# Kernel tuning notes

Hardware: AMD Instinct MI355X
Metric: run time of the kernel (lower is better)

The kernel has to match this reference:

```python
import jax, jax.numpy as jnp
import numpy as np

EMBED_DIM = 768
NUM_HEADS = 12
EPS = 1e-6


def setup_inputs() -> dict:
    key = jax.random.key(0)
    ks = jax.random.split(key, 9)
    B, C, H, W = 8, EMBED_DIM, 48, 48
    std = 0.02
    E = EMBED_DIM
    return {
        "query": jax.random.normal(ks[0], (B, C, H, W), dtype=jnp.float32),
        "Wq": jax.random.normal(ks[1], (E, E), dtype=jnp.float32) * std,
        "bq": jnp.zeros((E,), dtype=jnp.float32),
        "Wk": jax.random.normal(ks[2], (E, E), dtype=jnp.float32) * std,
        "bk": jnp.zeros((E,), dtype=jnp.float32),
        "Wv": jax.random.normal(ks[3], (E, E), dtype=jnp.float32) * std,
        "bv": jnp.zeros((E,), dtype=jnp.float32),
        "Wo": jax.random.normal(ks[4], (E, E), dtype=jnp.float32) * std,
        "bo": jnp.zeros((E,), dtype=jnp.float32),
    }


def reference(query, Wq, bq, Wk, bk, Wv, bv, Wo, bo):
    # query: (B, C, H, W) -> (L, B, E) with L = H*W
    B, C, H, W = query.shape
    L = H * W
    E = C
    h = NUM_HEADS
    d = E // h
    x = query.reshape(B, C, L).transpose(2, 0, 1)  # (L, B, E)

    # cos/sin positional reweighting: pi/2 * (i+1) / L
    idx = (jnp.pi / 2) * jnp.arange(1, L + 1, dtype=x.dtype) / L
    sin = jnp.sin(idx)[None, :, None]  # (1, L, 1)
    cos = jnp.cos(idx)[None, :, None]

    # projections + relu feature map
    q = jax.nn.relu(x @ Wq.T + bq)
    k = jax.nn.relu(x @ Wk.T + bk)
    v = x @ Wv.T + bv

    def to_heads(t):  # (L, B, E) -> (B*h, L, d)
        return t.reshape(L, B * h, d).transpose(1, 0, 2)

    q, k, v = to_heads(q), to_heads(k), to_heads(v)

    q_ = jnp.concatenate([q * sin, q * cos], axis=-1)  # (n, L, 2d)
    k_ = jnp.concatenate([k * sin, k * cos], axis=-1)

    # non-causal linear attention
    kv = jnp.einsum("nld,nlm->ndm", k_, v)              # (n, 2d, d)
    z = 1.0 / jnp.maximum(jnp.einsum("nld,nd->nl", q_, k_.sum(axis=1)), EPS)
    out = jnp.einsum("nld,ndm,nl->nlm", q_, kv, z)       # (n, L, d)

    # residual (DropPath is identity at inference)
    attn = x + out.transpose(1, 0, 2).reshape(L, B, E)
    return attn @ Wo.T + bo
```

## Files before the change

### kernel.cpp

```cpp
#include <hip/hip_runtime.h>


#define L_SEQ 2304
#define BATCH 8
#define EDIM 768
#define NHEAD 12
#define DHEAD 64
#define MROWS (L_SEQ * BATCH)

typedef __attribute__((ext_vector_type(8))) short bf16x8_t;
typedef __attribute__((ext_vector_type(4))) float f32x4_t;

__device__ __forceinline__ float b2f(unsigned short u) {
  union { unsigned int i; float f; } x; x.i = ((unsigned int)u) << 16; return x.f;
}
__device__ __forceinline__ unsigned short f2b(float f) {
  union { float f; unsigned int i; } x; x.f = f;
  unsigned int r = x.i + 0x7FFFu + ((x.i >> 16) & 1u);
  return (unsigned short)(r >> 16);
}

#define GLOAD_LDS16(g, l)                                                     \
  __builtin_amdgcn_global_load_lds(                                           \
      (const __attribute__((address_space(1))) unsigned int*)(g),             \
      (__attribute__((address_space(3))) unsigned int*)(l), 16, 0, 0)

__global__ __launch_bounds__(256) void prep(
    const float* __restrict__ q,
    const float* __restrict__ W0, const float* __restrict__ W1,
    const float* __restrict__ W2, const float* __restrict__ W3,
    unsigned short* __restrict__ wbf, unsigned short* __restrict__ xT,
    float* __restrict__ kvz, float2* __restrict__ sct) {
  __shared__ float tile[64][65];
  int bx = blockIdx.x;
  int t = threadIdx.x;
  if (bx < 2304) {
    int y = bx / 576;
    const float* W = (y == 0) ? W0 : (y == 1) ? W1 : (y == 2) ? W2 : W3;
    unsigned short* d = wbf + (size_t)y * EDIM * EDIM;
    int idx = (bx - y * 576) * 256 + t;
    float4 v = *(const float4*)(W + (size_t)idx * 4);
    ushort4 o;
    o.x = f2b(v.x); o.y = f2b(v.y); o.z = f2b(v.z); o.w = f2b(v.w);
    *(ushort4*)(d + (size_t)idx * 4) = o;
  } else if (bx < 5760) {
    int bb = bx - 2304;
    int e0 = (bb % 12) * 64;
    int l0 = ((bb / 12) % 36) * 64;
    int b = bb / 432;
    int li = t & 63, er = t >> 6;
#pragma unroll
    for (int p = 0; p < 16; p++) {
      int eo = er + p * 4;
      tile[eo][li] = q[((size_t)b * EDIM + (e0 + eo)) * L_SEQ + (l0 + li)];
    }
    __syncthreads();
    int ei = t & 63, lr = t >> 6;
#pragma unroll
    for (int p = 0; p < 16; p++) {
      int lo = lr + p * 4;
      xT[((size_t)b * L_SEQ + (l0 + lo)) * EDIM + (e0 + ei)] = f2b(tile[ei][lo]);
    }
  } else if (bx < 6540) {
    int idx = (bx - 5760) * 256 + t;
    *(float4*)(kvz + (size_t)idx * 4) = make_float4(0.f, 0.f, 0.f, 0.f);
  } else {
    int l = (bx - 6540) * 256 + t;
    if (l < L_SEQ) {
      float sv, cv;
      sincosf(1.5707963267948966f * (float)(l + 1) / 2304.0f, &sv, &cv);
      sct[l] = make_float2(sv, cv);
    }
  }
}

#define ABUF(b_) ((b_) * 8192)
#define BBUF(b_) (16384 + (b_) * 8192)

#define BAR() __builtin_amdgcn_s_barrier()
#define SB0() __builtin_amdgcn_sched_barrier(0)
#define LGKM0() asm volatile("s_waitcnt lgkmcnt(0)")
#define VMW(N) asm volatile("s_waitcnt vmcnt(" #N ")" ::: "memory")

#define STG_AB(kt_, B_)                                                       \
  {                                                                           \
    GLOAD_LDS16(a_sb + (size_t)(kt_) * 64, lds + ABUF(B_) + t * 8);           \
    GLOAD_LDS16(a_sb + (size_t)64 * EDIM + (size_t)(kt_) * 64,                \
                lds + ABUF(B_) + 4096 + t * 8);                               \
    GLOAD_LDS16(b_sb + (size_t)(kt_) * 64, lds + BBUF(B_) + t * 8);           \
    GLOAD_LDS16(b_sb + (size_t)64 * EDIM + (size_t)(kt_) * 64,                \
                lds + BBUF(B_) + 4096 + t * 8);                               \
  }

#define DS_RD(B_)                                                             \
  _Pragma("unroll") for (int m_ = 0; m_ < 4; m_++)                            \
  _Pragma("unroll") for (int kk_ = 0; kk_ < 2; kk_++)                         \
    aF[m_][kk_] = *(const bf16x8_t*)(lds + ABUF(B_) +                         \
        ((a_base + (m_ >> 1) * 4096 + (m_ & 1) * 1024 + kk_ * 32) ^ xorv));   \
  _Pragma("unroll") for (int n_ = 0; n_ < 2; n_++)                            \
  _Pragma("unroll") for (int kk_ = 0; kk_ < 2; kk_++)                         \
    bF[n_][kk_] = *(const bf16x8_t*)(lds + BBUF(B_) +                         \
        ((b_base + n_ * 4096 + kk_ * 32) ^ xorv));

#define MFMA16()                                                              \
  __builtin_amdgcn_s_setprio(1);                                              \
  _Pragma("unroll") for (int m_ = 0; m_ < 4; m_++)                            \
  _Pragma("unroll") for (int n_ = 0; n_ < 2; n_++)                            \
  _Pragma("unroll") for (int kk_ = 0; kk_ < 2; kk_++)                         \
    acc[m_][n_] = __builtin_amdgcn_mfma_f32_16x16x32_bf16(                    \
        aF[m_][kk_], bF[n_][kk_], acc[m_][n_], 0, 0, 0);                      \
  __builtin_amdgcn_s_setprio(0);

template <int MODE>
__global__ __launch_bounds__(512, 4) void gemm256(
    const unsigned short* __restrict__ A,
    const unsigned short* __restrict__ Wall,
    const float* __restrict__ bias0, const float* __restrict__ bias1,
    const float* __restrict__ bias2,
    unsigned short* __restrict__ dst0, unsigned short* __restrict__ dst1,
    unsigned short* __restrict__ dst2,
    float* __restrict__ dstf) {
  extern __shared__ __align__(16) unsigned short lds[];

  const unsigned short* W;
  const float* bias;
  unsigned short* dst = nullptr;
  bool do_relu = false;
  int rowblk, colblk;
  {
    int nwg = (int)gridDim.x;
    int wg = ((int)blockIdx.x & 7) * (nwg >> 3) + ((int)blockIdx.x >> 3);
    if (MODE == 0) {
      rowblk = wg / 18;
      int c = wg - rowblk * 18;
      colblk = c % 6;
      int z = c / 6;
      W = Wall + (size_t)z * EDIM * EDIM;
      bias = (z == 0) ? bias0 : (z == 1) ? bias1 : bias2;
      dst = (z == 0) ? dst0 : (z == 1) ? dst1 : dst2;
      do_relu = (z < 2);
    } else {
      rowblk = wg / 6;
      colblk = wg - rowblk * 6;
      W = Wall;
      bias = bias0;
    }
  }
  const int row0 = rowblk * 128;
  const int col0 = colblk * 128;

  const int t = threadIdx.x;
  const int lane = t & 63;
  const int wave = t >> 6;
  const int wm = wave >> 2;
  const int wn = wave & 3;
  const int mrow = lane & 15;
  const int quad = lane >> 4;

  const int xorv = (mrow & 7) << 3;
  const int a_base = (wm * 32 + mrow) * 64 + quad * 8;
  const int b_base = (wn * 16 + mrow) * 64 + quad * 8;

  const int lr_s = t >> 3;
  const int k0_s = ((((t >> 3) & 7) ^ (t & 7)) << 3);
  const unsigned short* a_sb = A + (size_t)(row0 + lr_s) * EDIM + k0_s;
  const unsigned short* b_sb = W + (size_t)(col0 + lr_s) * EDIM + k0_s;

  f32x4_t acc[4][2] = {};
  bf16x8_t aF[4][2], bF[2][2];

  STG_AB(0, 0);
  STG_AB(1, 1);
  VMW(4);
  BAR();

#pragma unroll
  for (int i = 0; i < 12; ++i) {
    const int cur = i & 1;
    DS_RD(cur);
    SB0();
    LGKM0();
    BAR();
    if (i < 10) STG_AB(i + 2, cur);
    MFMA16();
    if (i < 10) { VMW(4); } else { VMW(0); }
    BAR();
  }

  const int bb = row0 / L_SEQ;
#pragma unroll
  for (int ti = 0; ti < 4; ti++) {
    int rbase = row0 + (ti >> 1) * 64 + wm * 32 + (ti & 1) * 16 + quad * 4;
#pragma unroll
    for (int tj = 0; tj < 2; tj++) {
      int gc = col0 + tj * 64 + wn * 16 + mrow;
      float bv = bias[gc];
#pragma unroll
      for (int r = 0; r < 4; r++) {
        int gr = rbase + r;
        float v = acc[ti][tj][r] + bv;
        if (MODE == 0) {
          if (do_relu) v = fmaxf(v, 0.0f);
          int ll = gr - bb * L_SEQ;
          int n = bb * NHEAD + (gc >> 6);
          dst[((size_t)n * L_SEQ + ll) * DHEAD + (gc & 63)] = f2b(v);
        } else {
          dstf[(size_t)gr * EDIM + gc] = v;
        }
      }
    }
  }
}

__global__ __launch_bounds__(256) void kv_mfma(
    const unsigned short* __restrict__ kbuf, const unsigned short* __restrict__ vbuf,
    const float2* __restrict__ sct,
    float* __restrict__ kvT, float* __restrict__ ksum) {
  constexpr int ST = 40;
  __shared__ __align__(16) unsigned short ksT[128 * ST];
  __shared__ __align__(16) unsigned short vsT[64 * ST];
  __shared__ float ksum_l[128];
  int n = blockIdx.x;
  int lbase = blockIdx.y * 288;
  int t = threadIdx.x;
  int lane = t & 63, wave = t >> 6;
  int mrow = lane & 15, quad = lane >> 4;

  if (t < 128) ksum_l[t] = 0.f;

  int lrd = t >> 3;
  int oct = t & 7;
  int col2 = (lrd + ((oct & 3) << 3)) & 31;
  const unsigned short* kbase = kbuf + (size_t)n * L_SEQ * DHEAD + oct * 8;
  const unsigned short* vbase = vbuf + (size_t)n * L_SEQ * DHEAD + oct * 8;

  int rv = wave * 16 + mrow;
  const unsigned short* vrd = vsT + rv * ST + (((quad + (rv >> 3)) & 3) << 3);

  f32x4_t acc[8] = {};
  float sks[8] = {}, skc[8] = {};

  for (int s = 0; s < 9; s++) {
    int l = lbase + s * 32 + lrd;
    float2 sc = sct[l];
    union { uint4 q; unsigned short u[8]; } kq, vq;
    kq.q = *(const uint4*)(kbase + (size_t)l * DHEAD);
    vq.q = *(const uint4*)(vbase + (size_t)l * DHEAD);
    __syncthreads();
#pragma unroll
    for (int e = 0; e < 8; e++) {
      int d = oct * 8 + e;
      float kval = b2f(kq.u[e]);
      float a = kval * sc.x, c = kval * sc.y;
      ksT[d * ST + col2] = f2b(a);
      ksT[(64 + d) * ST + col2] = f2b(c);
      vsT[d * ST + col2] = vq.u[e];
      sks[e] += a;
      skc[e] += c;
    }
    __syncthreads();
    bf16x8_t af = *(const bf16x8_t*)(vrd);
#pragma unroll
    for (int jt = 0; jt < 8; jt++) {
      int rk = jt * 16 + mrow;
      bf16x8_t bfk = *(const bf16x8_t*)(ksT + rk * ST + (((quad + (rk >> 3)) & 3) << 3));
      acc[jt] = __builtin_amdgcn_mfma_f32_16x16x32_bf16(af, bfk, acc[jt], 0, 0, 0);
    }
  }

#pragma unroll
  for (int e = 0; e < 8; e++) {
    atomicAdd(&ksum_l[oct * 8 + e], sks[e]);
    atomicAdd(&ksum_l[64 + oct * 8 + e], skc[e]);
  }
  __syncthreads();
  if (t < 128) atomicAdd(&ksum[n * 128 + t], ksum_l[t]);

#pragma unroll
  for (int jt = 0; jt < 8; jt++) {
#pragma unroll
    for (int r = 0; r < 4; r++) {
      int m = wave * 16 + quad * 4 + r;
      int j = jt * 16 + mrow;
      atomicAdd(&kvT[((size_t)n * 64 + m) * 128 + j], acc[jt][r]);
    }
  }
}

__global__ __launch_bounds__(256) void attn_mfma(
    const unsigned short* __restrict__ qbuf, const float* __restrict__ kvT,
    const float* __restrict__ ksum, const unsigned short* __restrict__ xT,
    const float2* __restrict__ sct,
    unsigned short* __restrict__ attn) {
  __shared__ __align__(16) unsigned short As[128 * 72];
  __shared__ __align__(16) unsigned short Bs[64 * 136];
  __shared__ float ks_l[128];
  __shared__ float zs[128], zc[128];
  int l0 = blockIdx.x * 128;
  int n = blockIdx.y;
  int t = threadIdx.x;
  int lane = t & 63, wave = t >> 6;
  int mrow = lane & 15, quad = lane >> 4;
  int b = n / NHEAD, hd = n % NHEAD;

  {
    int row = t >> 1, off = (t & 1) * 32;
    const unsigned short* src = qbuf + ((size_t)n * L_SEQ + l0 + row) * DHEAD + off;
    unsigned short* d = As + row * 72 + off;
#pragma unroll
    for (int c = 0; c < 4; c++)
      *(uint4*)(d + c * 8) = *(const uint4*)(src + c * 8);
  }
  {
    int m = t >> 2, part = t & 3;
    const float* src = kvT + ((size_t)n * 64 + m) * 128 + part * 32;
    unsigned short* dBs = Bs + m * 136 + part * 32;
#pragma unroll
    for (int c = 0; c < 4; c++) {
      float4 a = *(const float4*)(src + c * 8);
      float4 bq = *(const float4*)(src + c * 8 + 4);
      ushort4 o1, o2;
      o1.x = f2b(a.x); o1.y = f2b(a.y); o1.z = f2b(a.z); o1.w = f2b(a.w);
      o2.x = f2b(bq.x); o2.y = f2b(bq.y); o2.z = f2b(bq.z); o2.w = f2b(bq.w);
      *(ushort4*)(dBs + c * 8) = o1;
      *(ushort4*)(dBs + c * 8 + 4) = o2;
    }
  }
  if (t < 128) ks_l[t] = ksum[n * 128 + t];
  __syncthreads();

  if (t < 128) {
    float d0 = 0.f, d1 = 0.f;
    const unsigned short* arow = As + t * 72;
#pragma unroll
    for (int j = 0; j < 8; j++) {
      bf16x8_t v = *(const bf16x8_t*)(arow + j * 8);
#pragma unroll
      for (int e = 0; e < 8; e++) {
        float qv = b2f((unsigned short)v[e]);
        d0 += qv * ks_l[j * 8 + e];
        d1 += qv * ks_l[64 + j * 8 + e];
      }
    }
    float2 sc = sct[l0 + t];
    float z = 1.0f / fmaxf(sc.x * d0 + sc.y * d1, 1e-6f);
    zs[t] = z * sc.x;
    zc[t] = z * sc.y;
  }
  __syncthreads();

  int wr = wave * 32;
  f32x4_t acc0[2][4] = {}, acc1[2][4] = {};
#pragma unroll
  for (int ks = 0; ks < 2; ks++) {
    bf16x8_t af[2];
#pragma unroll
    for (int ti = 0; ti < 2; ti++)
      af[ti] = *(const bf16x8_t*)(As + (wr + ti * 16 + mrow) * 72 + ks * 32 + quad * 8);
#pragma unroll
    for (int tj = 0; tj < 4; tj++) {
      bf16x8_t b0 = *(const bf16x8_t*)(Bs + (tj * 16 + mrow) * 136 + ks * 32 + quad * 8);
      bf16x8_t b1 = *(const bf16x8_t*)(Bs + (tj * 16 + mrow) * 136 + 64 + ks * 32 + quad * 8);
#pragma unroll
      for (int ti = 0; ti < 2; ti++) {
        acc0[ti][tj] = __builtin_amdgcn_mfma_f32_16x16x32_bf16(af[ti], b0, acc0[ti][tj], 0, 0, 0);
        acc1[ti][tj] = __builtin_amdgcn_mfma_f32_16x16x32_bf16(af[ti], b1, acc1[ti][tj], 0, 0, 0);
      }
    }
  }

#pragma unroll
  for (int ti = 0; ti < 2; ti++) {
#pragma unroll
    for (int tj = 0; tj < 4; tj++) {
      int m = tj * 16 + mrow;
#pragma unroll
      for (int r = 0; r < 4; r++) {
        int row = wr + ti * 16 + quad * 4 + r;
        int l = l0 + row;
        float ov = zs[row] * acc0[ti][tj][r] + zc[row] * acc1[ti][tj][r];
        float xv = b2f(xT[((size_t)b * L_SEQ + l) * EDIM + hd * DHEAD + m]);
        attn[((size_t)l * BATCH + b) * EDIM + hd * DHEAD + m] = f2b(xv + ov);
      }
    }
  }
}

extern "C" void kernel_launch(void* const* d_in, const int* in_sizes, int n_in,
                              void* d_out, int out_size, void* d_ws, size_t ws_size,
                              hipStream_t stream) {
  const float* query = (const float*)d_in[0];
  const float* Wq = (const float*)d_in[1];
  const float* bq = (const float*)d_in[2];
  const float* Wk = (const float*)d_in[3];
  const float* bk = (const float*)d_in[4];
  const float* Wv = (const float*)d_in[5];
  const float* bv = (const float*)d_in[6];
  const float* Wo = (const float*)d_in[7];
  const float* bo = (const float*)d_in[8];
  float* out = (float*)d_out;

  unsigned short* xT = (unsigned short*)d_out;

  char* ws = (char*)d_ws;
  const size_t SZ = (size_t)MROWS * EDIM * 2;
  unsigned short* qbuf = (unsigned short*)(ws);
  unsigned short* kbuf = (unsigned short*)(ws + SZ);
  unsigned short* vbuf = (unsigned short*)(ws + 2 * SZ);
  unsigned short* attn = kbuf;
  float* kvT  = (float*)(ws + 3 * SZ);
  float* ksum = (float*)(ws + 3 * SZ + 3145728);
  unsigned short* wbf = (unsigned short*)(ws + 3 * SZ + 3145728 + 49152);

  float2* sct = (float2*)((char*)d_out + SZ);

  static bool attr_done = false;
  if (!attr_done) {
    (void)hipFuncSetAttribute((const void*)gemm256<0>,
                              hipFuncAttributeMaxDynamicSharedMemorySize, 65536);
    (void)hipFuncSetAttribute((const void*)gemm256<1>,
                              hipFuncAttributeMaxDynamicSharedMemorySize, 65536);
    attr_done = true;
  }

  prep<<<dim3(6549), 256, 0, stream>>>(query, Wq, Wk, Wv, Wo, wbf, xT, kvT, sct);

  gemm256<0><<<dim3(2592), dim3(512), 65536, stream>>>(
      xT, wbf, bq, bk, bv, qbuf, kbuf, vbuf, nullptr);

  kv_mfma<<<dim3(96, 8), 256, 0, stream>>>(kbuf, vbuf, sct, kvT, ksum);

  attn_mfma<<<dim3(L_SEQ / 128, 96), 256, 0, stream>>>(qbuf, kvT, ksum, xT, sct, attn);

  gemm256<1><<<dim3(864), dim3(512), 65536, stream>>>(
      attn, wbf + 3 * (size_t)EDIM * EDIM, bo, nullptr, nullptr,
      nullptr, nullptr, nullptr, out);
}
```

Baseline: 307.2 us.

## Fuse K/V projection GEMM with KV reduction to skip materializing K and V

Result: slower. 322.3 us (+4.9%).

```diff
diff --git a/kernel.cpp b/kernel.cpp
--- a/kernel.cpp
+++ b/kernel.cpp
@@ -24,6 +24,12 @@
   __builtin_amdgcn_global_load_lds(                                           \
       (const __attribute__((address_space(1))) unsigned int*)(g),             \
       (__attribute__((address_space(3))) unsigned int*)(l), 16, 0, 0)
+
+#define BAR() __builtin_amdgcn_s_barrier()
+#define SB0() __builtin_amdgcn_sched_barrier(0)
+#define LGKM0() asm volatile("s_waitcnt lgkmcnt(0)")
+#define LGKM0M() asm volatile("s_waitcnt lgkmcnt(0)" ::: "memory")
+#define VMW(N) asm volatile("s_waitcnt vmcnt(" #N ")" ::: "memory")
 
 __global__ __launch_bounds__(256) void prep(
     const float* __restrict__ q,
@@ -77,11 +83,6 @@
 #define ABUF(b_) ((b_) * 8192)
 #define BBUF(b_) (16384 + (b_) * 8192)
 
-#define BAR() __builtin_amdgcn_s_barrier()
-#define SB0() __builtin_amdgcn_sched_barrier(0)
-#define LGKM0() asm volatile("s_waitcnt lgkmcnt(0)")
-#define VMW(N) asm volatile("s_waitcnt vmcnt(" #N ")" ::: "memory")
-
 #define STG_AB(kt_, B_)                                                       \
   {                                                                           \
     GLOAD_LDS16(a_sb + (size_t)(kt_) * 64, lds + ABUF(B_) + t * 8);           \
@@ -114,37 +115,18 @@
 template <int MODE>
 __global__ __launch_bounds__(512, 4) void gemm256(
     const unsigned short* __restrict__ A,
-    const unsigned short* __restrict__ Wall,
-    const float* __restrict__ bias0, const float* __restrict__ bias1,
-    const float* __restrict__ bias2,
-    unsigned short* __restrict__ dst0, unsigned short* __restrict__ dst1,
-    unsigned short* __restrict__ dst2,
+    const unsigned short* __restrict__ W,
+    const float* __restrict__ bias,
+    unsigned short* __restrict__ dstb,
     float* __restrict__ dstf) {
   extern __shared__ __align__(16) unsigned short lds[];
 
-  const unsigned short* W;
-  const float* bias;
-  unsigned short* dst = nullptr;
-  bool do_relu = false;
   int rowblk, colblk;
   {
     int nwg = (int)gridDim.x;
     int wg = ((int)blockIdx.x & 7) * (nwg >> 3) + ((int)blockIdx.x >> 3);
-    if (MODE == 0) {
-      rowblk = wg / 18;
-      int c = wg - rowblk * 18;
-      colblk = c % 6;
-      int z = c / 6;
-      W = Wall + (size_t)z * EDIM * EDIM;
-      bias = (z == 0) ? bias0 : (z == 1) ? bias1 : bias2;
-      dst = (z == 0) ? dst0 : (z == 1) ? dst1 : dst2;
-      do_relu = (z < 2);
-    } else {
-      rowblk = wg / 6;
-      colblk = wg - rowblk * 6;
-      W = Wall;
-      bias = bias0;
-    }
+    rowblk = wg / 6;
+    colblk = wg - rowblk * 6;
   }
   const int row0 = rowblk * 128;
   const int col0 = colblk * 128;
@@ -200,10 +182,10 @@
         int gr = rbase + r;
         float v = acc[ti][tj][r] + bv;
         if (MODE == 0) {
-          if (do_relu) v = fmaxf(v, 0.0f);
+          v = fmaxf(v, 0.0f);
           int ll = gr - bb * L_SEQ;
           int n = bb * NHEAD + (gc >> 6);
-          dst[((size_t)n * L_SEQ + ll) * DHEAD + (gc & 63)] = f2b(v);
+          dstb[((size_t)n * L_SEQ + ll) * DHEAD + (gc & 63)] = f2b(v);
         } else {
           dstf[(size_t)gr * EDIM + gc] = v;
         }
@@ -212,77 +194,165 @@
   }
 }
 
-__global__ __launch_bounds__(256) void kv_mfma(
-    const unsigned short* __restrict__ kbuf, const unsigned short* __restrict__ vbuf,
+#define KAB(b_) ((b_) * 8192)
+#define KBB(b_) (16384 + (b_) * 8192)
+#define KST 32768
+#define VST 41984
+#define ST2 72
+
+#define KSTG(srow_, kt_, B_)                                                  \
+  {                                                                           \
+    GLOAD_LDS16(a_sb + (size_t)(srow_) * EDIM + (kt_) * 64,                   \
+                lds + KAB(B_) + t * 8);                                       \
+    GLOAD_LDS16(a_sb + (size_t)((srow_) + 64) * EDIM + (kt_) * 64,            \
+                lds + KAB(B_) + 4096 + t * 8);                                \
+    GLOAD_LDS16(wk_sb + (kt_) * 64, lds + KBB(B_) + t * 8);                   \
+    GLOAD_LDS16(wv_sb + (kt_) * 64, lds + KBB(B_) + 4096 + t * 8);            \
+  }
+
+#define KDS_RD(B_)                                                            \
+  _Pragma("unroll") for (int m_ = 0; m_ < 4; m_++)                            \
+  _Pragma("unroll") for (int kk_ = 0; kk_ < 2; kk_++)                         \
+    aF[m_][kk_] = *(const bf16x8_t*)(lds + KAB(B_) +                          \
+        ((a_base + (m_ >> 1) * 4096 + (m_ & 1) * 1024 + kk_ * 32) ^ xorv));   \
+  _Pragma("unroll") for (int n_ = 0; n_ < 2; n_++)                            \
+  _Pragma("unroll") for (int kk_ = 0; kk_ < 2; kk_++)                         \
+    bF[n_][kk_] = *(const bf16x8_t*)(lds + KBB(B_) +                          \
+        ((b_base + n_ * 4096 + kk_ * 32) ^ xorv));
+
+__global__ __launch_bounds__(512, 2) void kv_fused(
+    const unsigned short* __restrict__ xT, const unsigned short* __restrict__ wbf,
+    const float* __restrict__ bk, const float* __restrict__ bv,
     const float2* __restrict__ sct,
     float* __restrict__ kvT, float* __restrict__ ksum) {
-  constexpr int ST = 40;
-  __shared__ __align__(16) unsigned short ksT[128 * ST];
-  __shared__ __align__(16) unsigned short vsT[64 * ST];
-  __shared__ float ksum_l[128];
-  int n = blockIdx.x;
-  int lbase = blockIdx.y * 288;
-  int t = threadIdx.x;
-  int lane = t & 63, wave = t >> 6;
-  int mrow = lane & 15, quad = lane >> 4;
+  extern __shared__ __align__(16) unsigned short lds[];
+  float* ksum_l = (float*)(lds + 46592);
+
+  int bx = blockIdx.x;
+  int n = bx / 3, c = bx - n * 3;
+  int b = n / NHEAD, hd = n % NHEAD;
+
+  const int t = threadIdx.x;
+  const int lane = t & 63;
+  const int wave = t >> 6;
+  const int wm = wave >> 2;
+  const int wn = wave & 3;
+  const int mrow = lane & 15;
+  const int quad = lane >> 4;
+
+  const int xorv = (mrow & 7) << 3;
+  const int a_base = (wm * 32 + mrow) * 64 + quad * 8;
+  const int b_base = (wn * 16 + mrow) * 64 + quad * 8;
+
+  const int lr_s = t >> 3;
+  const int k0_s = ((((t >> 3) & 7) ^ (t & 7)) << 3);
+  const unsigned short* a_sb =
+      xT + ((size_t)(b * L_SEQ + c * 768) + lr_s) * EDIM + k0_s;
+  const unsigned short* wk_sb =
+      wbf + (size_t)EDIM * EDIM + (size_t)(hd * 64 + lr_s) * EDIM + k0_s;
+  const unsigned short* wv_sb =
+      wbf + (size_t)2 * EDIM * EDIM + (size_t)(hd * 64 + lr_s) * EDIM + k0_s;
+
+  const int colh = wn * 16 + mrow;
+  const float bkv = bk[hd * 64 + colh];
+  const float bvv = bv[hd * 64 + colh];
 
   if (t < 128) ksum_l[t] = 0.f;
 
-  int lrd = t >> 3;
-  int oct = t & 7;
-  int col2 = (lrd + ((oct & 3) << 3)) & 31;
-  const unsigned short* kbase = kbuf + (size_t)n * L_SEQ * DHEAD + oct * 8;
-  const unsigned short* vbase = vbuf + (size_t)n * L_SEQ * DHEAD + oct * 8;
-
-  int rv = wave * 16 + mrow;
-  const unsigned short* vrd = vsT + rv * ST + (((quad + (rv >> 3)) & 3) << 3);
-
-  f32x4_t acc[8] = {};
-  float sks[8] = {}, skc[8] = {};
-
-  for (int s = 0; s < 9; s++) {
-    int l = lbase + s * 32 + lrd;
-    float2 sc = sct[l];
-    union { uint4 q; unsigned short u[8]; } kq, vq;
-    kq.q = *(const uint4*)(kbase + (size_t)l * DHEAD);
-    vq.q = *(const uint4*)(vbase + (size_t)l * DHEAD);
-    __syncthreads();
-#pragma unroll
-    for (int e = 0; e < 8; e++) {
-      int d = oct * 8 + e;
-      float kval = b2f(kq.u[e]);
-      float a = kval * sc.x, c = kval * sc.y;
-      ksT[d * ST + col2] = f2b(a);
-      ksT[(64 + d) * ST + col2] = f2b(c);
-      vsT[d * ST + col2] = vq.u[e];
-      sks[e] += a;
-      skc[e] += c;
-    }
-    __syncthreads();
-    bf16x8_t af = *(const bf16x8_t*)(vrd);
-#pragma unroll
-    for (int jt = 0; jt < 8; jt++) {
-      int rk = jt * 16 + mrow;
-      bf16x8_t bfk = *(const bf16x8_t*)(ksT + rk * ST + (((quad + (rk >> 3)) & 3) << 3));
-      acc[jt] = __builtin_amdgcn_mfma_f32_16x16x32_bf16(af, bfk, acc[jt], 0, 0, 0);
-    }
-  }
-
-#pragma unroll
-  for (int e = 0; e < 8; e++) {
-    atomicAdd(&ksum_l[oct * 8 + e], sks[e]);
-    atomicAdd(&ksum_l[64 + oct * 8 + e], skc[e]);
-  }
+  const int mt = wave & 3;
+  const int j0 = (wave >> 2) * 4;
+  f32x4_t accKV[4] = {};
+  float sks = 0.f, skc = 0.f;
+
+  bf16x8_t aF[4][2], bF[2][2];
+
+  KSTG(0, 0, 0);
+  KSTG(0, 1, 1);
+  VMW(4);
+  BAR();
+
+  for (int lt = 0; lt < 6; lt++) {
+    f32x4_t acc[4][2] = {};
+#pragma unroll
+    for (int i = 0; i < 12; ++i) {
+      const int cur = i & 1;
+      KDS_RD(cur);
+      SB0();
+      LGKM0();
+      BAR();
+      const bool stg = (lt < 5) || (i < 10);
+      if (stg) {
+        int srow = ((i < 10) ? lt : (lt + 1)) * 128;
+        const int skt = (i + 2) % 12;
+        KSTG(srow, skt, cur);
+      }
+      MFMA16();
+      if (stg) { VMW(4); } else { VMW(0); }
+      BAR();
+    }
+
+#pragma unroll
+    for (int sl = 0; sl < 2; sl++) {
+#pragma unroll
+      for (int mi = 0; mi < 2; mi++) {
+        const int m_ = sl * 2 + mi;
+        const int lrow = wm * 32 + mi * 16 + quad * 4;
+        const int gl = c * 768 + lt * 128 + sl * 64 + lrow;
+        ushort4 pks, pkc, pv;
+#pragma unroll
+        for (int r = 0; r < 4; r++) {
+          float2 sc = sct[gl + r];
+          float kvl = fmaxf(acc[m_][0][r] + bkv, 0.f);
+          float a = kvl * sc.x, cc = kvl * sc.y;
+          sks += a; skc += cc;
+          ((unsigned short*)&pks)[r] = f2b(a);
+          ((unsigned short*)&pkc)[r] = f2b(cc);
+          ((unsigned short*)&pv)[r] = f2b(acc[m_][1][r] + bvv);
+        }
+        *(ushort4*)(lds + KST + (colh * ST2 + lrow)) = pks;
+        *(ushort4*)(lds + KST + ((64 + colh) * ST2 + lrow)) = pkc;
+        *(ushort4*)(lds + VST + (colh * ST2 + lrow)) = pv;
+      }
+      SB0();
+      LGKM0M();
+      BAR();
+      SB0();
+      {
+        bf16x8_t av[2];
+#pragma unroll
+        for (int kk = 0; kk < 2; kk++)
+          av[kk] = *(const bf16x8_t*)(lds + VST +
+                                      ((mt * 16 + mrow) * ST2 + kk * 32 + quad * 8));
+#pragma unroll
+        for (int jj = 0; jj < 4; jj++) {
+#pragma unroll
+          for (int kk = 0; kk < 2; kk++) {
+            bf16x8_t bk8 = *(const bf16x8_t*)(lds + KST +
+                (((j0 + jj) * 16 + mrow) * ST2 + kk * 32 + quad * 8));
+            accKV[jj] = __builtin_amdgcn_mfma_f32_16x16x32_bf16(
+                av[kk], bk8, accKV[jj], 0, 0, 0);
+          }
+        }
+      }
+      SB0();
+      LGKM0M();
+      BAR();
+      SB0();
+    }
+  }
+
+  atomicAdd(&ksum_l[colh], sks);
+  atomicAdd(&ksum_l[64 + colh], skc);
   __syncthreads();
   if (t < 128) atomicAdd(&ksum[n * 128 + t], ksum_l[t]);
 
 #pragma unroll
-  for (int jt = 0; jt < 8; jt++) {
+  for (int jj = 0; jj < 4; jj++) {
 #pragma unroll
     for (int r = 0; r < 4; r++) {
-      int m = wave * 16 + quad * 4 + r;
-      int j = jt * 16 + mrow;
-      atomicAdd(&kvT[((size_t)n * 64 + m) * 128 + j], acc[jt][r]);
+      int m = mt * 16 + quad * 4 + r;
+      int j = (j0 + jj) * 16 + mrow;
+      atomicAdd(&kvT[((size_t)n * 64 + m) * 128 + j], accKV[jj][r]);
     }
   }
 }
@@ -405,9 +475,7 @@
   char* ws = (char*)d_ws;
   const size_t SZ = (size_t)MROWS * EDIM * 2;
   unsigned short* qbuf = (unsigned short*)(ws);
-  unsigned short* kbuf = (unsigned short*)(ws + SZ);
-  unsigned short* vbuf = (unsigned short*)(ws + 2 * SZ);
-  unsigned short* attn = kbuf;
+  unsigned short* attnb = (unsigned short*)(ws + SZ);
   float* kvT  = (float*)(ws + 3 * SZ);
   float* ksum = (float*)(ws + 3 * SZ + 3145728);
   unsigned short* wbf = (unsigned short*)(ws + 3 * SZ + 3145728 + 49152);
@@ -420,19 +488,19 @@
                               hipFuncAttributeMaxDynamicSharedMemorySize, 65536);
     (void)hipFuncSetAttribute((const void*)gemm256<1>,
                               hipFuncAttributeMaxDynamicSharedMemorySize, 65536);
+    (void)hipFuncSetAttribute((const void*)kv_fused,
+                              hipFuncAttributeMaxDynamicSharedMemorySize, 93696);
     attr_done = true;
   }
 
   prep<<<dim3(6549), 256, 0, stream>>>(query, Wq, Wk, Wv, Wo, wbf, xT, kvT, sct);
 
-  gemm256<0><<<dim3(2592), dim3(512), 65536, stream>>>(
-      xT, wbf, bq, bk, bv, qbuf, kbuf, vbuf, nullptr);
-
-  kv_mfma<<<dim3(96, 8), 256, 0, stream>>>(kbuf, vbuf, sct, kvT, ksum);
-
-  attn_mfma<<<dim3(L_SEQ / 128, 96), 256, 0, stream>>>(qbuf, kvT, ksum, xT, sct, attn);
+  gemm256<0><<<dim3(864), dim3(512), 65536, stream>>>(xT, wbf, bq, qbuf, nullptr);
+
+  kv_fused<<<dim3(288), dim3(512), 93696, stream>>>(xT, wbf, bk, bv, sct, kvT, ksum);
+
+  attn_mfma<<<dim3(L_SEQ / 128, 96), 256, 0, stream>>>(qbuf, kvT, ksum, xT, sct, attnb);
 
   gemm256<1><<<dim3(864), dim3(512), 65536, stream>>>(
-      attn, wbf + 3 * (size_t)EDIM * EDIM, bo, nullptr, nullptr,
-      nullptr, nullptr, nullptr, out);
-}
+      attnb, wbf + 3 * (size_t)EDIM * EDIM, bo, nullptr, out);
+}
```
